# Optimization experiments

Hardware: AMD Instinct MI355X
Metric: run time of the kernel (lower is better)

## Reference

```python
import jax, jax.numpy as jnp
import numpy as np

N_NODES = 65536
N_EDGES = 655360
IN_C = 128
OUT_C = 64
K_HOPS = 2


def setup_inputs() -> dict:
    key = jax.random.key(0)
    k1, k2, k3 = jax.random.split(key, 3)
    x = jax.random.normal(k1, (N_NODES, IN_C), dtype=jnp.float32)
    edge_index = jax.random.randint(k2, (2, N_EDGES), 0, N_NODES, dtype=jnp.int32)
    # SGConv's terminal Linear(in_c, out_c): weight [out_c, in_c], bias [out_c]
    W = jax.random.normal(k3, (OUT_C, IN_C), dtype=jnp.float32) * 0.05
    b = jnp.zeros((OUT_C,), dtype=jnp.float32)
    return {"x": x, "edge_index": edge_index, "W": W, "b": b}


def reference(x, edge_index, W, b):
    n = x.shape[0]
    loop = jnp.arange(n, dtype=edge_index.dtype)
    # gcn_norm with added self-loops (edge weight 1)
    src = jnp.concatenate([edge_index[0], loop])  # message sources
    dst = jnp.concatenate([edge_index[1], loop])  # aggregation targets
    deg = jax.ops.segment_sum(jnp.ones_like(src, dtype=x.dtype), dst, num_segments=n)
    dinv = jax.lax.rsqrt(deg)  # deg >= 1 thanks to self-loops
    norm = (dinv[src] * dinv[dst])[:, None]  # [E+N, 1]
    # K repeated sparse propagations: h <- D^{-1/2}(A+I)D^{-1/2} h
    h = x
    for _ in range(K_HOPS):
        h = jax.ops.segment_sum(norm * h[src], dst, num_segments=n)
    # terminal dense linear
    return h @ W.T + b
```

## Files before the change

### kernel.cpp

```cpp
#include <hip/hip_runtime.h>

#define IN_C 128
#define OUT_C 64
#define PAD 8
#define GP 132
typedef long long ll;


__global__ __launch_bounds__(256) void k_fused_gc(const float* __restrict__ x,
                                                  const float* __restrict__ W,
                                                  float* __restrict__ y0,
                                                  const int* __restrict__ dst,
                                                  int* __restrict__ cnt,
                                                  int nGemm, int E) {
    if ((int)blockIdx.x >= nGemm) {
        int e = (blockIdx.x - nGemm) * 256 + threadIdx.x;
        if (e < E) atomicAdd(&cnt[dst[e]], 1);
        return;
    }
    __shared__ float xs[64 * GP];
    int tid  = threadIdx.x;
    int lane = tid & 63;
    int wid  = tid >> 6;
    int r0   = blockIdx.x << 6;

    float4 wreg[32];
    const float4* W4 = (const float4*)(W + (ll)lane * IN_C);
    #pragma unroll
    for (int q = 0; q < 32; ++q) wreg[q] = W4[q];

    #pragma unroll
    for (int k = 0; k < 8; ++k) {
        int fidx = tid + k * 256;
        int row  = fidx >> 5;
        int c4   = (fidx & 31) << 2;
        float4 v = *(const float4*)(x + (ll)(r0 + row) * IN_C + c4);
        *(float4*)&xs[row * GP + c4] = v;
    }
    __syncthreads();

    #pragma unroll
    for (int rr = 0; rr < 16; ++rr) {
        int row = (wid << 4) + rr;
        const float4* xq = (const float4*)&xs[row * GP];
        float a0 = 0.f, a1 = 0.f, a2 = 0.f, a3 = 0.f;
        #pragma unroll
        for (int q = 0; q < 32; ++q) {
            float4 xv = xq[q];
            float4 wv = wreg[q];
            a0 += xv.x * wv.x; a1 += xv.y * wv.y;
            a2 += xv.z * wv.z; a3 += xv.w * wv.w;
        }
        y0[(ll)(r0 + row) * OUT_C + lane] = (a0 + a1) + (a2 + a3);
    }
}


__global__ __launch_bounds__(256) void k_alloc(int* __restrict__ cnt_cursor,
                                               int4* __restrict__ meta,
                                               float* __restrict__ dinv,
                                               int2* __restrict__ wcol,
                                               int* __restrict__ total, int N) {
    int i    = blockIdx.x * 256 + threadIdx.x;
    int lane = threadIdx.x & 63;
    int c  = (i < N) ? cnt_cursor[i] : 0;
    int c8 = (c + PAD - 1) & ~(PAD - 1);
    int scan = c8;
    #pragma unroll
    for (int d = 1; d < 64; d <<= 1) {
        int t = __shfl_up(scan, d);
        if (lane >= d) scan += t;
    }
    int wave_total = __shfl(scan, 63);
    int base = 0;
    if (lane == 63) base = atomicAdd(total, wave_total);
    base = __shfl(base, 63);
    if (i < N) {
        int s = base + scan - c8;
        float dv = 1.0f / sqrtf((float)(c + 1));
        meta[i] = make_int4(s, c8, __float_as_int(dv), 0);
        dinv[i] = dv;
        cnt_cursor[i] = s;
        for (int p = s + c; p < s + c8; ++p)
            wcol[p] = make_int2(i, 0);
    }
}

__global__ __launch_bounds__(256) void k_fill(const int* __restrict__ src,
                                              const int* __restrict__ dst,
                                              int* __restrict__ cursor,
                                              const float* __restrict__ dinv,
                                              int2* __restrict__ wcol, int E) {
    int e = blockIdx.x * 256 + threadIdx.x;
    if (e < E) {
        int s = src[e], d = dst[e];
        int p = atomicAdd(&cursor[d], 1);
        float w = dinv[s] * dinv[d];
        wcol[p] = make_int2(s, __float_as_int(w));
    }
}


template<int G>
__device__ __forceinline__ void g8(float& a0, float& a1, const float* __restrict__ hin,
                                   int2 slot, int lane) {
    int j[8]; float w[8];
    #pragma unroll
    for (int k = 0; k < 8; ++k) {
        j[k] = __builtin_amdgcn_readlane(slot.x, G + k);
        w[k] = __int_as_float(__builtin_amdgcn_readlane(slot.y, G + k));
    }
    float u[8];
    #pragma unroll
    for (int k = 0; k < 8; ++k) u[k] = hin[(ll)j[k] * OUT_C + lane];
    #pragma unroll
    for (int k = 0; k < 8; ++k) { if (k & 1) a1 += w[k] * u[k]; else a0 += w[k] * u[k]; }
}

__device__ __forceinline__ void g8dyn(float& a0, float& a1, const float* __restrict__ hin,
                                      int2 slot, int g, int lane) {
    int j[8]; float w[8];
    #pragma unroll
    for (int k = 0; k < 8; ++k) {
        j[k] = __builtin_amdgcn_readlane(slot.x, g + k);
        w[k] = __int_as_float(__builtin_amdgcn_readlane(slot.y, g + k));
    }
    float u[8];
    #pragma unroll
    for (int k = 0; k < 8; ++k) u[k] = hin[(ll)j[k] * OUT_C + lane];
    #pragma unroll
    for (int k = 0; k < 8; ++k) { if (k & 1) a1 += w[k] * u[k]; else a0 += w[k] * u[k]; }
}

__device__ __forceinline__ float gather64(const float* __restrict__ hin,
                                          const int2* __restrict__ wcol,
                                          int s, int c8, float di, int i, int lane) {
    float v  = hin[(ll)i * OUT_C + lane];
    float a0 = di * di * v, a1 = 0.f;
    if (c8 == 8) {
        int2 sl = wcol[s + lane];
        g8<0>(a0, a1, hin, sl, lane);
    } else if (c8 == 16) {
        int2 sl = wcol[s + lane];
        g8<0>(a0, a1, hin, sl, lane);
        g8<8>(a0, a1, hin, sl, lane);
    } else if (c8 > 0) {
        for (int base = 0; base < c8; base += 64) {
            int nb = min(64, c8 - base);
            int2 sl = wcol[s + base + lane];
            for (int g = 0; g < nb; g += 8) g8dyn(a0, a1, hin, sl, g, lane);
        }
    }
    return a0 + a1;
}

__global__ __launch_bounds__(256) void k_hop64(const float* __restrict__ hin,
                                               const int2* __restrict__ wcol,
                                               const int4* __restrict__ meta,
                                               float* __restrict__ hout, int N) {
    int lane = threadIdx.x & 63;
    int w0 = (blockIdx.x * blockDim.x + threadIdx.x) >> 6;
    int nw = (gridDim.x * blockDim.x) >> 6;
    for (int ii = w0; ii < N; ii += nw) {
        int i = __builtin_amdgcn_readfirstlane(ii);
        int4 m = meta[i];
        float acc = gather64(hin, wcol, m.x, m.y, __int_as_float(m.z), i, lane);
        hout[(ll)i * OUT_C + lane] = acc;
    }
}

__global__ __launch_bounds__(256) void k_hop64_bias(const float* __restrict__ hin,
                                                    const int2* __restrict__ wcol,
                                                    const int4* __restrict__ meta,
                                                    const float* __restrict__ b,
                                                    float* __restrict__ out, int N) {
    int lane = threadIdx.x & 63;
    int w0 = (blockIdx.x * blockDim.x + threadIdx.x) >> 6;
    int nw = (gridDim.x * blockDim.x) >> 6;
    float bias = b[lane];
    for (int ii = w0; ii < N; ii += nw) {
        int i = __builtin_amdgcn_readfirstlane(ii);
        int4 m = meta[i];
        float acc = gather64(hin, wcol, m.x, m.y, __int_as_float(m.z), i, lane);
        out[(ll)i * OUT_C + lane] = acc + bias;
    }
}


extern "C" void kernel_launch(void* const* d_in, const int* in_sizes, int n_in,
                              void* d_out, int out_size, void* d_ws, size_t ws_size,
                              hipStream_t stream) {
    const float* x  = (const float*)d_in[0];
    const int*   ei = (const int*)d_in[1];
    const float* W  = (const float*)d_in[2];
    const float* b  = (const float*)d_in[3];
    float* out = (float*)d_out;

    int N = in_sizes[0] / IN_C;
    int E = in_sizes[1] / 2;
    const int* src = ei;
    const int* dst = ei + E;

    size_t cap_slots = (size_t)E + (size_t)PAD * N + 64;
    size_t off_total = (size_t)N * 4;
    size_t off_meta  = ((off_total + 4 + 255) & ~(size_t)255);
    size_t off_dinv  = off_meta + (size_t)N * 16;
    size_t off_wcol  = off_dinv + (size_t)N * 4;
    size_t off_y0    = ((off_wcol + cap_slots * 8 + 255) & ~(size_t)255);
    size_t off_h1    = off_y0 + (size_t)N * OUT_C * 4;
    size_t need      = off_h1 + (size_t)N * OUT_C * 4;
    if (ws_size < need) return;

    char* ws = (char*)d_ws;
    int*   cnt_cursor = (int*)(ws);
    int*   total      = (int*)(ws + off_total);
    int4*  meta       = (int4*)(ws + off_meta);
    float* dinv       = (float*)(ws + off_dinv);
    int2*  wcol       = (int2*)(ws + off_wcol);
    float* y0         = (float*)(ws + off_y0);
    float* h1         = (float*)(ws + off_h1);

    hipMemsetAsync(ws, 0, off_total + 4, stream);

    int nGemm  = N >> 6;
    int nCount = (E + 255) / 256;
    int gn     = (N + 255) / 256;

    k_fused_gc<<<nGemm + nCount, 256, 0, stream>>>(x, W, y0, dst, cnt_cursor, nGemm, E);
    k_alloc   <<<gn, 256, 0, stream>>>(cnt_cursor, meta, dinv, wcol, total, N);
    k_fill    <<<nCount, 256, 0, stream>>>(src, dst, cnt_cursor, dinv, wcol, E);

    k_hop64     <<<4096, 256, 0, stream>>>(y0, wcol, meta, h1, N);
    k_hop64_bias<<<4096, 256, 0, stream>>>(h1, wcol, meta, b, out, N);
}
```

Measured before the change: 229.5 us.

## Interleave two destination rows per wave in hop gathers; drop LDS staging in GEMM

The hop kernels now have each wave process two destination nodes at once. Gather loads for both nodes are issued before either is accumulated, which doubles the memory-level parallelism per wave and helps hide gather latency. The fused GEMM no longer stages x tiles in shared memory with a barrier. Each wave instead reads its 16 rows straight from global memory with a smaller unroll. The trade-offs are higher register pressure, a more complex control path, and possibly less coalesced x reads in the GEMM.

```diff
diff --git a/kernel.cpp b/kernel.cpp
--- a/kernel.cpp
+++ b/kernel.cpp
@@ -3,7 +3,6 @@
 #define IN_C 128
 #define OUT_C 64
 #define PAD 8
-#define GP 132
 typedef long long ll;
 
 
@@ -18,31 +17,19 @@
         if (e < E) atomicAdd(&cnt[dst[e]], 1);
         return;
     }
-    __shared__ float xs[64 * GP];
     int tid  = threadIdx.x;
     int lane = tid & 63;
     int wid  = tid >> 6;
-    int r0   = blockIdx.x << 6;
+    int r0   = (blockIdx.x << 6) + (wid << 4);
 
     float4 wreg[32];
     const float4* W4 = (const float4*)(W + (ll)lane * IN_C);
     #pragma unroll
     for (int q = 0; q < 32; ++q) wreg[q] = W4[q];
 
-    #pragma unroll
-    for (int k = 0; k < 8; ++k) {
-        int fidx = tid + k * 256;
-        int row  = fidx >> 5;
-        int c4   = (fidx & 31) << 2;
-        float4 v = *(const float4*)(x + (ll)(r0 + row) * IN_C + c4);
-        *(float4*)&xs[row * GP + c4] = v;
-    }
-    __syncthreads();
-
-    #pragma unroll
+    #pragma unroll 2
     for (int rr = 0; rr < 16; ++rr) {
-        int row = (wid << 4) + rr;
-        const float4* xq = (const float4*)&xs[row * GP];
+        const float4* xq = (const float4*)(x + (ll)(r0 + rr) * IN_C);
         float a0 = 0.f, a1 = 0.f, a2 = 0.f, a3 = 0.f;
         #pragma unroll
         for (int q = 0; q < 32; ++q) {
@@ -51,7 +38,7 @@
             a0 += xv.x * wv.x; a1 += xv.y * wv.y;
             a2 += xv.z * wv.z; a3 += xv.w * wv.w;
         }
-        y0[(ll)(r0 + row) * OUT_C + lane] = (a0 + a1) + (a2 + a3);
+        y0[(ll)(r0 + rr) * OUT_C + lane] = (a0 + a1) + (a2 + a3);
     }
 }
 
@@ -101,35 +88,25 @@
 }
 
 
-template<int G>
-__device__ __forceinline__ void g8(float& a0, float& a1, const float* __restrict__ hin,
-                                   int2 slot, int lane) {
-    int j[8]; float w[8];
+struct G8 { float u[8]; float w[8]; };
+
+__device__ __forceinline__ void g8_issue(G8& g, const float* __restrict__ hin,
+                                         int2 slot, int off, int lane) {
+    int j[8];
     #pragma unroll
     for (int k = 0; k < 8; ++k) {
-        j[k] = __builtin_amdgcn_readlane(slot.x, G + k);
-        w[k] = __int_as_float(__builtin_amdgcn_readlane(slot.y, G + k));
-    }
-    float u[8];
-    #pragma unroll
-    for (int k = 0; k < 8; ++k) u[k] = hin[(ll)j[k] * OUT_C + lane];
-    #pragma unroll
-    for (int k = 0; k < 8; ++k) { if (k & 1) a1 += w[k] * u[k]; else a0 += w[k] * u[k]; }
-}
-
-__device__ __forceinline__ void g8dyn(float& a0, float& a1, const float* __restrict__ hin,
-                                      int2 slot, int g, int lane) {
-    int j[8]; float w[8];
+        j[k]   = __builtin_amdgcn_readlane(slot.x, off + k);
+        g.w[k] = __int_as_float(__builtin_amdgcn_readlane(slot.y, off + k));
+    }
+    #pragma unroll
+    for (int k = 0; k < 8; ++k) g.u[k] = hin[(ll)j[k] * OUT_C + lane];
+}
+
+__device__ __forceinline__ void g8_acc(const G8& g, float& a0, float& a1) {
     #pragma unroll
     for (int k = 0; k < 8; ++k) {
-        j[k] = __builtin_amdgcn_readlane(slot.x, g + k);
-        w[k] = __int_as_float(__builtin_amdgcn_readlane(slot.y, g + k));
-    }
-    float u[8];
-    #pragma unroll
-    for (int k = 0; k < 8; ++k) u[k] = hin[(ll)j[k] * OUT_C + lane];
-    #pragma unroll
-    for (int k = 0; k < 8; ++k) { if (k & 1) a1 += w[k] * u[k]; else a0 += w[k] * u[k]; }
+        if (k & 1) a1 += g.w[k] * g.u[k]; else a0 += g.w[k] * g.u[k];
+    }
 }
 
 __device__ __forceinline__ float gather64(const float* __restrict__ hin,
@@ -137,21 +114,63 @@
                                           int s, int c8, float di, int i, int lane) {
     float v  = hin[(ll)i * OUT_C + lane];
     float a0 = di * di * v, a1 = 0.f;
-    if (c8 == 8) {
-        int2 sl = wcol[s + lane];
-        g8<0>(a0, a1, hin, sl, lane);
-    } else if (c8 == 16) {
-        int2 sl = wcol[s + lane];
-        g8<0>(a0, a1, hin, sl, lane);
-        g8<8>(a0, a1, hin, sl, lane);
-    } else if (c8 > 0) {
-        for (int base = 0; base < c8; base += 64) {
-            int nb = min(64, c8 - base);
-            int2 sl = wcol[s + base + lane];
-            for (int g = 0; g < nb; g += 8) g8dyn(a0, a1, hin, sl, g, lane);
+    for (int base = 0; base < c8; base += 64) {
+        int nb = min(64, c8 - base);
+        int2 sl = wcol[s + base + lane];
+        for (int g = 0; g < nb; g += 8) {
+            G8 gg;
+            g8_issue(gg, hin, sl, g, lane);
+            g8_acc(gg, a0, a1);
         }
     }
     return a0 + a1;
+}
+
+__device__ __forceinline__ void hop_pair(const float* __restrict__ hin,
+                                         const int2* __restrict__ wcol,
+                                         const int4* __restrict__ meta,
+                                         float* __restrict__ hout,
+                                         int N, int w0, int nw, int lane, float bias) {
+    for (int ii = w0; ii < N; ii += 2 * nw) {
+        int iA = __builtin_amdgcn_readfirstlane(ii);
+        int ib = ii + nw;
+        if (ib < N) {
+            int iB = __builtin_amdgcn_readfirstlane(ib);
+            int4 mA = meta[iA];
+            int4 mB = meta[iB];
+            int sA = mA.x, c8A = mA.y; float dA = __int_as_float(mA.z);
+            int sB = mB.x, c8B = mB.y; float dB = __int_as_float(mB.z);
+            if (c8A <= 64 && c8B <= 64) {
+                int2 slA = wcol[sA + lane];
+                int2 slB = wcol[sB + lane];
+                float vA = hin[(ll)iA * OUT_C + lane];
+                float vB = hin[(ll)iB * OUT_C + lane];
+                float aA0 = dA * dA * vA, aA1 = 0.f;
+                float aB0 = dB * dB * vB, aB1 = 0.f;
+                int nA = c8A >> 3, nB = c8B >> 3;
+                int nmax = nA > nB ? nA : nB;
+                for (int t = 0; t < nmax; ++t) {
+                    G8 ga, gb;
+                    bool doA = t < nA, doB = t < nB;
+                    if (doA) g8_issue(ga, hin, slA, t << 3, lane);
+                    if (doB) g8_issue(gb, hin, slB, t << 3, lane);
+                    if (doA) g8_acc(ga, aA0, aA1);
+                    if (doB) g8_acc(gb, aB0, aB1);
+                }
+                hout[(ll)iA * OUT_C + lane] = aA0 + aA1 + bias;
+                hout[(ll)iB * OUT_C + lane] = aB0 + aB1 + bias;
+            } else {
+                float aA = gather64(hin, wcol, sA, c8A, dA, iA, lane);
+                float aB = gather64(hin, wcol, sB, c8B, dB, iB, lane);
+                hout[(ll)iA * OUT_C + lane] = aA + bias;
+                hout[(ll)iB * OUT_C + lane] = aB + bias;
+            }
+        } else {
+            int4 m = meta[iA];
+            float acc = gather64(hin, wcol, m.x, m.y, __int_as_float(m.z), iA, lane);
+            hout[(ll)iA * OUT_C + lane] = acc + bias;
+        }
+    }
 }
 
 __global__ __launch_bounds__(256) void k_hop64(const float* __restrict__ hin,
@@ -161,12 +180,7 @@
     int lane = threadIdx.x & 63;
     int w0 = (blockIdx.x * blockDim.x + threadIdx.x) >> 6;
     int nw = (gridDim.x * blockDim.x) >> 6;
-    for (int ii = w0; ii < N; ii += nw) {
-        int i = __builtin_amdgcn_readfirstlane(ii);
-        int4 m = meta[i];
-        float acc = gather64(hin, wcol, m.x, m.y, __int_as_float(m.z), i, lane);
-        hout[(ll)i * OUT_C + lane] = acc;
-    }
+    hop_pair(hin, wcol, meta, hout, N, w0, nw, lane, 0.f);
 }
 
 __global__ __launch_bounds__(256) void k_hop64_bias(const float* __restrict__ hin,
@@ -177,13 +191,7 @@
     int lane = threadIdx.x & 63;
     int w0 = (blockIdx.x * blockDim.x + threadIdx.x) >> 6;
     int nw = (gridDim.x * blockDim.x) >> 6;
-    float bias = b[lane];
-    for (int ii = w0; ii < N; ii += nw) {
-        int i = __builtin_amdgcn_readfirstlane(ii);
-        int4 m = meta[i];
-        float acc = gather64(hin, wcol, m.x, m.y, __int_as_float(m.z), i, lane);
-        out[(ll)i * OUT_C + lane] = acc + bias;
-    }
+    hop_pair(hin, wcol, meta, out, N, w0, nw, lane, b[lane]);
 }
 
 
```

Result: slower. 316.2 us (+37.8%).
